# Optimization experiments

Measured on AMD Instinct MI355X. Metric: run time of the kernel, lower is better.

## Reference

```python
import jax, jax.numpy as jnp
import numpy as np

B, N, C = 128, 2048, 3
VL, PN = 256, 128  # vector_length, prediction_num
NEG_SLOPE = 0.01   # torch LeakyReLU default
BN_EPS = 1e-5


def _lin(key, fin, fout):
    k1, k2 = jax.random.split(key)
    lim = 1.0 / np.sqrt(fin)
    W = jax.random.uniform(k1, (fin, fout), minval=-lim, maxval=lim, dtype=jnp.float32)
    b = jax.random.uniform(k2, (fout,), minval=-lim, maxval=lim, dtype=jnp.float32)
    return W, b


def setup_inputs() -> dict:
    key = jax.random.key(0)
    ks = jax.random.split(key, 14)
    x = jax.random.normal(ks[0], (B, N, C), dtype=jnp.float32)
    lengths = jnp.maximum(jax.random.randint(ks[1], (B,), 0, N), 1).astype(jnp.int32)
    eps = jax.random.normal(ks[2], (B, VL), dtype=jnp.float32)
    W1, b1 = _lin(ks[3], C, 64)
    W2, b2 = _lin(ks[4], 64, 64)
    W3, b3 = _lin(ks[5], 64, 128)
    W4, b4 = _lin(ks[6], 128, 1024)
    Wf, bf = _lin(ks[7], 1024, 1024)
    Wmu, bmu = _lin(ks[8], 1024, VL)
    Wlv, blv = _lin(ks[9], 1024, VL)
    Wd1, bd1 = _lin(ks[10], VL, 1024)
    Wd2, bd2 = _lin(ks[11], 1024, 1024)
    Wd3, bd3 = _lin(ks[12], 1024, PN * C)
    g1 = jnp.ones((1024,), jnp.float32); be1 = jnp.zeros((1024,), jnp.float32)
    g2 = jnp.ones((1024,), jnp.float32); be2 = jnp.zeros((1024,), jnp.float32)
    return dict(x=x, lengths=lengths, eps=eps,
                W1=W1, b1=b1, W2=W2, b2=b2, W3=W3, b3=b3, W4=W4, b4=b4,
                Wf=Wf, bf=bf, Wmu=Wmu, bmu=bmu, Wlv=Wlv, blv=blv,
                Wd1=Wd1, bd1=bd1, g1=g1, be1=be1,
                Wd2=Wd2, bd2=bd2, g2=g2, be2=be2,
                Wd3=Wd3, bd3=bd3)


def _lrelu(h):
    return jnp.where(h > 0, h, NEG_SLOPE * h)


def _bn(h, g, b):
    # BatchNorm1d in training mode: biased batch stats
    m = h.mean(axis=0)
    v = h.var(axis=0)
    return (h - m) * jax.lax.rsqrt(v + BN_EPS) * g + b


def reference(x, lengths, eps,
              W1, b1, W2, b2, W3, b3, W4, b4,
              Wf, bf, Wmu, bmu, Wlv, blv,
              Wd1, bd1, g1, be1, Wd2, bd2, g2, be2, Wd3, bd3):
    # --- pointnet per-point MLP (batched over padded [B,N,C]) ---
    h = _lrelu(x @ W1 + b1)          # [B,N,64]
    h = _lrelu(h @ W2 + b2)          # [B,N,64]
    h = _lrelu(h @ W3 + b3)          # [B,N,128]
    h = _lrelu(h @ W4 + b4)          # [B,N,1024]
    # masked max over points (ragged -> padded+mask)
    mask = jnp.arange(N)[None, :] < lengths[:, None]   # [B,N]
    h = jnp.where(mask[:, :, None], h, -jnp.inf)
    pooled = jnp.max(h, axis=1)      # [B,1024]
    # --- encoder head ---
    e = _lrelu(pooled @ Wf + bf)
    mu = e @ Wmu + bmu               # [B,VL]
    logvar = e @ Wlv + blv           # [B,VL]
    # --- reparameterize ---
    z = mu + eps * jnp.exp(0.5 * logvar)
    # --- decoder: Linear+BN+LeakyReLU x2, final Linear ---
    d = _lrelu(_bn(z @ Wd1 + bd1, g1, be1))
    d = _lrelu(_bn(d @ Wd2 + bd2, g2, be2))
    y = (d @ Wd3 + bd3).reshape(-1, PN, C)   # [B,PN,C]
    return (y, mu, logvar)
```

## Files before the change

kernel.cpp:

```cpp
#include <hip/hip_runtime.h>
#include <hip/hip_bf16.h>
#include <math.h>

#define NEG_SLOPE 0.01f

typedef short short8 __attribute__((ext_vector_type(8)));
typedef float f32x4 __attribute__((ext_vector_type(4)));

__device__ __forceinline__ float lrelu(float v) { return v > 0.0f ? v : NEG_SLOPE * v; }

__device__ __forceinline__ short f2bf(float f) {
    __hip_bfloat16 h = __float2bfloat16(f);
    return __builtin_bit_cast(short, h);
}
__device__ __forceinline__ float bf2f(short s) {
    __hip_bfloat16 h = __builtin_bit_cast(__hip_bfloat16, s);
    return __bfloat162float(h);
}

__global__ __launch_bounds__(256) void pack_all(
    const float* __restrict__ W4, const float* __restrict__ Wf,
    const float* __restrict__ Wmu, const float* __restrict__ Wlv,
    const float* __restrict__ Wd1, const float* __restrict__ Wd2,
    const float* __restrict__ Wd3, const float* __restrict__ W2,
    const float* __restrict__ W3,
    short* __restrict__ F4, short* __restrict__ Ff, short* __restrict__ Fmuvl,
    short* __restrict__ Fd1, short* __restrict__ Fd2, short* __restrict__ Fd3,
    short* __restrict__ F2, short* __restrict__ F3)
{
    int bid = blockIdx.x;
    const float* src = nullptr; short* dst = nullptr; int K = 0, N = 0; int muvl = 0;
    if      (bid < 64)   { src = W4;  dst = F4;    K = 128;  N = 1024; }
    else if (bid < 576)  { src = Wf;  dst = Ff;    K = 1024; N = 1024; bid -= 64; }
    else if (bid < 832)  { src = nullptr; dst = Fmuvl; K = 1024; N = 512; muvl = 1; bid -= 576; }
    else if (bid < 960)  { src = Wd1; dst = Fd1;   K = 256;  N = 1024; bid -= 832; }
    else if (bid < 1472) { src = Wd2; dst = Fd2;   K = 1024; N = 1024; bid -= 960; }
    else if (bid < 1664) { src = Wd3; dst = Fd3;   K = 1024; N = 384;  bid -= 1472; }
    else if (bid < 1666) { src = W2;  dst = F2;    K = 64;   N = 64;   bid -= 1664; }
    else                 { src = W3;  dst = F3;    K = 64;   N = 128;  bid -= 1666; }

    const int fragid = bid * 4 + (threadIdx.x >> 6);
    const int lane   = threadIdx.x & 63;
    const int K32    = K >> 5;
    const int t   = fragid / (K32 * 4);
    const int rem = fragid - t * K32 * 4;
    const int ks  = rem >> 2;
    const int n   = rem & 3;
    const int col   = t * 64 + n * 16 + (lane & 15);
    const int kbase = ks * 32 + (lane >> 4) * 8;

    short8 v;
#pragma unroll
    for (int e = 0; e < 8; ++e) {
        float f;
        if (muvl) f = (col < 256) ? Wmu[(size_t)(kbase + e) * 256 + col]
                                  : Wlv[(size_t)(kbase + e) * 256 + col - 256];
        else      f = src[(size_t)(kbase + e) * N + col];
        v[e] = f2bf(f);
    }
    *(short8*)&dst[(size_t)fragid * 512 + lane * 8] = v;
}

__global__ __launch_bounds__(256, 2) void fused_pointnet_kernel(
    const float* __restrict__ x, const int* __restrict__ lengths,
    const float* __restrict__ W1, const float* __restrict__ b1,
    const float* __restrict__ b2, const float* __restrict__ b3,
    const short* __restrict__ F2, const short* __restrict__ F3,
    const short* __restrict__ F4,
    short* __restrict__ partials)
{
    const int tid = threadIdx.x;
    const int b   = blockIdx.x & 127;
    const int sc  = blockIdx.x >> 7;
    const int len = lengths[b];
    if (sc * 256 >= len) return;

    __shared__ short S[32768];
    const int lane = tid & 63;
    const int w    = tid >> 6;
    short* Aw = S + w * 8192;
    const int gid = b * 2048 + sc * 256 + tid;

    {
        const float x0 = x[gid * 3 + 0];
        const float x1 = x[gid * 3 + 1];
        const float x2 = x[gid * 3 + 2];
#pragma unroll
        for (int q = 0; q < 8; ++q) {
            short8 pv;
#pragma unroll
            for (int e = 0; e < 8; ++e) {
                int c = q * 8 + e;
                float v = b1[c];
                v = fmaf(x0, W1[c], v);
                v = fmaf(x1, W1[64 + c], v);
                v = fmaf(x2, W1[128 + c], v);
                pv[e] = f2bf(lrelu(v));
            }
            *(short8*)&Aw[lane * 64 + ((q ^ (lane & 7)) * 8)] = pv;
        }
    }

    {
        short8 a2[4][2];
#pragma unroll
        for (int m = 0; m < 4; ++m)
#pragma unroll
            for (int ks = 0; ks < 2; ++ks) {
                int rl = m * 16 + (lane & 15);
                int kch = ks * 4 + (lane >> 4);
                a2[m][ks] = *(const short8*)&Aw[rl * 64 + ((kch ^ (rl & 7)) * 8)];
            }
        short8 b2f[2][4];
#pragma unroll
        for (int ks = 0; ks < 2; ++ks)
#pragma unroll
            for (int n = 0; n < 4; ++n)
                b2f[ks][n] = *(const short8*)&F2[(size_t)(ks * 4 + n) * 512 + lane * 8];

        f32x4 acc2[4][4];
#pragma unroll
        for (int m = 0; m < 4; ++m)
#pragma unroll
            for (int n = 0; n < 4; ++n) acc2[m][n] = 0;
#pragma unroll
        for (int ks = 0; ks < 2; ++ks)
#pragma unroll
            for (int n = 0; n < 4; ++n)
#pragma unroll
                for (int m = 0; m < 4; ++m)
                    acc2[m][n] = __builtin_amdgcn_mfma_f32_16x16x32_bf16(
                        a2[m][ks], b2f[ks][n], acc2[m][n], 0, 0, 0);

#pragma unroll
        for (int n = 0; n < 4; ++n) {
            int col = n * 16 + (lane & 15);
            float bv = b2[col];
            int colch = col >> 3;
#pragma unroll
            for (int m = 0; m < 4; ++m)
#pragma unroll
                for (int r = 0; r < 4; ++r) {
                    int rl = m * 16 + (lane >> 4) * 4 + r;
                    Aw[4096 + rl * 64 + ((colch ^ (rl & 7)) * 8) + (col & 7)] =
                        f2bf(lrelu(acc2[m][n][r] + bv));
                }
        }
    }

    {
        short8 a3[4][2];
#pragma unroll
        for (int m = 0; m < 4; ++m)
#pragma unroll
            for (int ks = 0; ks < 2; ++ks) {
                int rl = m * 16 + (lane & 15);
                int kch = ks * 4 + (lane >> 4);
                a3[m][ks] = *(const short8*)&Aw[4096 + rl * 64 + ((kch ^ (rl & 7)) * 8)];
            }
#pragma unroll
        for (int half = 0; half < 2; ++half) {
            short8 b3f[2][4];
#pragma unroll
            for (int ks = 0; ks < 2; ++ks)
#pragma unroll
                for (int n = 0; n < 4; ++n)
                    b3f[ks][n] = *(const short8*)&F3[(size_t)(half * 8 + ks * 4 + n) * 512 + lane * 8];

            f32x4 acc3[4][4];
#pragma unroll
            for (int m = 0; m < 4; ++m)
#pragma unroll
                for (int n = 0; n < 4; ++n) acc3[m][n] = 0;
#pragma unroll
            for (int ks = 0; ks < 2; ++ks)
#pragma unroll
                for (int n = 0; n < 4; ++n)
#pragma unroll
                    for (int m = 0; m < 4; ++m)
                        acc3[m][n] = __builtin_amdgcn_mfma_f32_16x16x32_bf16(
                            a3[m][ks], b3f[ks][n], acc3[m][n], 0, 0, 0);

#pragma unroll
            for (int n = 0; n < 4; ++n) {
                int col = half * 64 + n * 16 + (lane & 15);
                float bv = b3[col];
                int colch = col >> 3;
#pragma unroll
                for (int m = 0; m < 4; ++m)
#pragma unroll
                    for (int r = 0; r < 4; ++r) {
                        int rl = m * 16 + (lane >> 4) * 4 + r;
                        Aw[rl * 128 + ((colch ^ (rl & 7)) * 8) + (col & 7)] =
                            f2bf(lrelu(acc3[m][n][r] + bv));
                    }
            }
        }
    }

    short8 af[4][4];
#pragma unroll
    for (int m = 0; m < 4; ++m)
#pragma unroll
        for (int ks = 0; ks < 4; ++ks) {
            int rl = m * 16 + (lane & 15);
            int ch = (ks * 4 + (lane >> 4)) ^ (rl & 7);
            af[m][ks] = *(const short8*)&Aw[rl * 128 + ch * 8];
        }

    const bool full = (sc * 256 + 256) <= len;
    float madd[4][4];
    if (!full) {
#pragma unroll
        for (int m = 0; m < 4; ++m)
#pragma unroll
            for (int r = 0; r < 4; ++r) {
                int rloc = sc * 256 + w * 64 + m * 16 + (lane >> 4) * 4 + r;
                madd[m][r] = (rloc < len) ? 0.0f : -INFINITY;
            }
    }

    short8 stg[4];
#pragma unroll
    for (int i = 0; i < 4; ++i)
        stg[i] = *(const short8*)&F4[w * 2048 + i * 512 + lane * 8];

    __syncthreads();
#pragma unroll
    for (int i = 0; i < 4; ++i)
        *(short8*)&S[w * 2048 + i * 512 + lane * 8] = stg[i];

    for (int t = 0; t < 16; ++t) {
        __syncthreads();
        if (t < 15) {
#pragma unroll
            for (int i = 0; i < 4; ++i)
                stg[i] = *(const short8*)&F4[(size_t)(t + 1) * 8192 + w * 2048 + i * 512 + lane * 8];
        }

        const short* Bb = S + (t & 1) * 8192;
        f32x4 acc[4][4];
#pragma unroll
        for (int m = 0; m < 4; ++m)
#pragma unroll
            for (int n = 0; n < 4; ++n) acc[m][n] = 0;

#pragma unroll
        for (int ks = 0; ks < 4; ++ks) {
            short8 bfr[4];
#pragma unroll
            for (int n = 0; n < 4; ++n)
                bfr[n] = *(const short8*)&Bb[(ks * 4 + n) * 512 + lane * 8];
#pragma unroll
            for (int n = 0; n < 4; ++n)
#pragma unroll
                for (int m = 0; m < 4; ++m)
                    acc[m][n] = __builtin_amdgcn_mfma_f32_16x16x32_bf16(
                        af[m][ks], bfr[n], acc[m][n], 0, 0, 0);
        }

        const size_t pb = ((size_t)((b * 8 + sc) * 4 + w)) * 1024 + t * 64;
#pragma unroll
        for (int n = 0; n < 4; ++n) {
            float v;
            if (full) {
                v = acc[0][n][0];
#pragma unroll
                for (int m = 0; m < 4; ++m)
#pragma unroll
                    for (int r = 0; r < 4; ++r)
                        if (m | r) v = fmaxf(v, acc[m][n][r]);
            } else {
                v = -INFINITY;
#pragma unroll
                for (int m = 0; m < 4; ++m)
#pragma unroll
                    for (int r = 0; r < 4; ++r)
                        v = fmaxf(v, acc[m][n][r] + madd[m][r]);
            }
            v = fmaxf(v, __shfl_xor(v, 16));
            v = fmaxf(v, __shfl_xor(v, 32));
            if (lane < 16) partials[pb + n * 16 + lane] = f2bf(v);
        }

        if (t < 15) {
            short* Bn = S + ((t + 1) & 1) * 8192;
#pragma unroll
            for (int i = 0; i < 4; ++i)
                *(short8*)&Bn[w * 2048 + i * 512 + lane * 8] = stg[i];
        }
    }
}

__global__ __launch_bounds__(256) void reduce_pool_kernel(
    const short* __restrict__ partials, const int* __restrict__ lengths,
    const float* __restrict__ b4, short* __restrict__ pooled)
{
    const int b = blockIdx.x;
    const int nlive = (lengths[b] + 255) >> 8;
    for (int i = threadIdx.x; i < 1024; i += 256) {
        float m = -INFINITY;
        for (int j = 0; j < nlive; ++j) {
#pragma unroll
            for (int w = 0; w < 4; ++w)
                m = fmaxf(m, bf2f(partials[((size_t)((b * 8 + j) * 4 + w)) * 1024 + i]));
        }
        pooled[(size_t)b * 1024 + i] = f2bf(lrelu(m + b4[i]));
    }
}

template<int MF, int K32>
__global__ __launch_bounds__(256) void gemm_tail(
    const short* __restrict__ A, const short* __restrict__ Wfrag,
    const float* __restrict__ bias,
    const float* __restrict__ g, const float* __restrict__ be,
    float* __restrict__ outF, short* __restrict__ outB,
    int Nout, int flags)
{
    __shared__ float bns[4][32];
    __shared__ float bnq[4][32];

    const int tid = threadIdx.x, lane = tid & 63, w = tid >> 6;
    const int K   = K32 * 32;
    const int c0  = blockIdx.x * 32;
    const int tt  = blockIdx.x >> 1;
    const int hf  = blockIdx.x & 1;
    const int row0  = (MF == 2) ? 0 : blockIdx.y * 64;
    const int arow0 = row0 + w * (MF * 16) + (lane & 15);
    const int koff  = (lane >> 4) * 8;

    f32x4 acc[MF][2];
#pragma unroll
    for (int m = 0; m < MF; ++m) { acc[m][0] = 0; acc[m][1] = 0; }

#pragma unroll
    for (int ks = 0; ks < K32; ++ks) {
        short8 a[MF], bfr[2];
#pragma unroll
        for (int m = 0; m < MF; ++m)
            a[m] = *(const short8*)&A[(size_t)(arow0 + m * 16) * K + ks * 32 + koff];
#pragma unroll
        for (int n = 0; n < 2; ++n)
            bfr[n] = *(const short8*)&Wfrag[(size_t)((tt * K32 + ks) * 4 + hf * 2 + n) * 512 + lane * 8];
#pragma unroll
        for (int n = 0; n < 2; ++n)
#pragma unroll
            for (int m = 0; m < MF; ++m)
                acc[m][n] = __builtin_amdgcn_mfma_f32_16x16x32_bf16(a[m], bfr[n], acc[m][n], 0, 0, 0);
    }

    if ((flags & 2) && MF == 2) {
#pragma unroll
        for (int n = 0; n < 2; ++n) {
            float s = 0.f, q = 0.f;
#pragma unroll
            for (int m = 0; m < MF; ++m)
#pragma unroll
                for (int r = 0; r < 4; ++r) {
                    float v = acc[m][n][r];
                    s += v; q = fmaf(v, v, q);
                }
            s += __shfl_xor(s, 16); s += __shfl_xor(s, 32);
            q += __shfl_xor(q, 16); q += __shfl_xor(q, 32);
            if (lane < 16) { bns[w][n * 16 + lane] = s; bnq[w][n * 16 + lane] = q; }
        }
        __syncthreads();
#pragma unroll
        for (int n = 0; n < 2; ++n) {
            int cl = n * 16 + (lane & 15);
            float s = bns[0][cl] + bns[1][cl] + bns[2][cl] + bns[3][cl];
            float q = bnq[0][cl] + bnq[1][cl] + bnq[2][cl] + bnq[3][cl];
            float mean = s * (1.0f / 128.0f);
            float var  = q * (1.0f / 128.0f) - mean * mean;
            float rs   = 1.0f / sqrtf(var + 1e-5f);
            float gg   = g[c0 + cl] * rs;
            float bb   = be[c0 + cl] - mean * gg;
#pragma unroll
            for (int m = 0; m < MF; ++m)
#pragma unroll
                for (int r = 0; r < 4; ++r)
                    acc[m][n][r] = fmaf(acc[m][n][r], gg, bb);
        }
    } else if (bias) {
#pragma unroll
        for (int n = 0; n < 2; ++n) {
            float bv = bias[c0 + n * 16 + (lane & 15)];
#pragma unroll
            for (int m = 0; m < MF; ++m)
#pragma unroll
                for (int r = 0; r < 4; ++r) acc[m][n][r] += bv;
        }
    }

    if (flags & 1) {
#pragma unroll
        for (int m = 0; m < MF; ++m)
#pragma unroll
            for (int n = 0; n < 2; ++n)
#pragma unroll
                for (int r = 0; r < 4; ++r) acc[m][n][r] = lrelu(acc[m][n][r]);
    }

#pragma unroll
    for (int m = 0; m < MF; ++m)
#pragma unroll
        for (int n = 0; n < 2; ++n)
#pragma unroll
            for (int r = 0; r < 4; ++r) {
                int row = row0 + w * (MF * 16) + m * 16 + (lane >> 4) * 4 + r;
                int col = c0 + n * 16 + (lane & 15);
                if (flags & 4) outB[(size_t)row * Nout + col] = f2bf(acc[m][n][r]);
                else           outF[(size_t)row * Nout + col] = acc[m][n][r];
            }
}

__global__ __launch_bounds__(256) void gemm_muvlz(
    const short* __restrict__ A, const short* __restrict__ Fmuvl,
    const float* __restrict__ bmu, const float* __restrict__ blv,
    const float* __restrict__ eps,
    float* __restrict__ mu_out, float* __restrict__ lv_out,
    short* __restrict__ zbuf)
{
    const int tid = threadIdx.x, lane = tid & 63, w = tid >> 6;
    const int c0 = blockIdx.x * 32;
    const int tt = blockIdx.x >> 1;
    const int hf = blockIdx.x & 1;
    const int row0 = blockIdx.y * 64;
    const int arow = row0 + w * 16 + (lane & 15);
    const int koff = (lane >> 4) * 8;

    f32x4 macc[2], lacc[2];
#pragma unroll
    for (int n = 0; n < 2; ++n) { macc[n] = 0; lacc[n] = 0; }

#pragma unroll
    for (int ks = 0; ks < 32; ++ks) {
        short8 a = *(const short8*)&A[(size_t)arow * 1024 + ks * 32 + koff];
#pragma unroll
        for (int n = 0; n < 2; ++n) {
            short8 bm = *(const short8*)&Fmuvl[(size_t)((tt * 32 + ks) * 4 + hf * 2 + n) * 512 + lane * 8];
            short8 bl = *(const short8*)&Fmuvl[(size_t)(((tt + 4) * 32 + ks) * 4 + hf * 2 + n) * 512 + lane * 8];
            macc[n] = __builtin_amdgcn_mfma_f32_16x16x32_bf16(a, bm, macc[n], 0, 0, 0);
            lacc[n] = __builtin_amdgcn_mfma_f32_16x16x32_bf16(a, bl, lacc[n], 0, 0, 0);
        }
    }

#pragma unroll
    for (int n = 0; n < 2; ++n) {
        int col = c0 + n * 16 + (lane & 15);
        float bmv = bmu[col], blvv = blv[col];
#pragma unroll
        for (int r = 0; r < 4; ++r) {
            int row = row0 + w * 16 + (lane >> 4) * 4 + r;
            float mu = macc[n][r] + bmv;
            float lv = lacc[n][r] + blvv;
            mu_out[(size_t)row * 256 + col] = mu;
            lv_out[(size_t)row * 256 + col] = lv;
            float z = fmaf(eps[(size_t)row * 256 + col], expf(0.5f * lv), mu);
            zbuf[(size_t)row * 256 + col] = f2bf(z);
        }
    }
}

extern "C" void kernel_launch(void* const* d_in, const int* in_sizes, int n_in,
                              void* d_out, int out_size, void* d_ws, size_t ws_size,
                              hipStream_t stream)
{
    const float* x       = (const float*)d_in[0];
    const int*   lengths = (const int*)  d_in[1];
    const float* eps     = (const float*)d_in[2];
    const float* W1  = (const float*)d_in[3];  const float* b1  = (const float*)d_in[4];
    const float* W2  = (const float*)d_in[5];  const float* b2  = (const float*)d_in[6];
    const float* W3  = (const float*)d_in[7];  const float* b3  = (const float*)d_in[8];
    const float* W4  = (const float*)d_in[9];  const float* b4  = (const float*)d_in[10];
    const float* Wf  = (const float*)d_in[11]; const float* bf  = (const float*)d_in[12];
    const float* Wmu = (const float*)d_in[13]; const float* bmu = (const float*)d_in[14];
    const float* Wlv = (const float*)d_in[15]; const float* blv = (const float*)d_in[16];
    const float* Wd1 = (const float*)d_in[17];
    const float* g1  = (const float*)d_in[19]; const float* be1 = (const float*)d_in[20];
    const float* Wd2 = (const float*)d_in[21];
    const float* g2  = (const float*)d_in[23]; const float* be2 = (const float*)d_in[24];
    const float* Wd3 = (const float*)d_in[25]; const float* bd3 = (const float*)d_in[26];

    float* out = (float*)d_out;
    float* y_out  = out;
    float* mu_out = out + 49152;
    float* lv_out = out + 81920;

    char* ws = (char*)d_ws;
    short* F4    = (short*)(ws + 0);
    short* Ff    = (short*)(ws + 262144);
    short* Fmuvl = (short*)(ws + 2359296);
    short* Fd1   = (short*)(ws + 3407872);
    short* Fd2   = (short*)(ws + 3932160);
    short* Fd3   = (short*)(ws + 6029312);
    short* F2    = (short*)(ws + 6815744);
    short* F3    = (short*)(ws + 6823936);
    short* partials = (short*)(ws + 6840320);
    short* pooled = (short*)(ws + 15228928);
    short* ebuf   = (short*)(ws + 15491072);
    short* zbuf   = (short*)(ws + 15753216);
    short* d1v    = (short*)(ws + 15818752);
    short* d2v    = (short*)(ws + 16080896);

    pack_all<<<1670, 256, 0, stream>>>(W4, Wf, Wmu, Wlv, Wd1, Wd2, Wd3, W2, W3,
                                       F4, Ff, Fmuvl, Fd1, Fd2, Fd3, F2, F3);
    fused_pointnet_kernel<<<1024, 256, 0, stream>>>(
        x, lengths, W1, b1, b2, b3, F2, F3, F4, partials);
    reduce_pool_kernel<<<128, 256, 0, stream>>>(partials, lengths, b4, pooled);
    gemm_tail<1, 32><<<dim3(32, 2), 256, 0, stream>>>(pooled, Ff, bf, nullptr, nullptr,
                                                      nullptr, ebuf, 1024, 1 | 4);
    gemm_muvlz<<<dim3(8, 2), 256, 0, stream>>>(ebuf, Fmuvl, bmu, blv, eps,
                                               mu_out, lv_out, zbuf);
    gemm_tail<2, 8><<<32, 256, 0, stream>>>(zbuf, Fd1, nullptr, g1, be1,
                                            nullptr, d1v, 1024, 1 | 2 | 4);
    gemm_tail<2, 32><<<32, 256, 0, stream>>>(d1v, Fd2, nullptr, g2, be2,
                                             nullptr, d2v, 1024, 1 | 2 | 4);
    gemm_tail<1, 32><<<dim3(12, 2), 256, 0, stream>>>(d2v, Fd3, bd3, nullptr, nullptr,
                                                      y_out, nullptr, 384, 0);
}
```

Before: 144.2 us.

## Split pointnet into h3 materialization and weight-stationary layer4 max-pool kernel

The fused per-point kernel is split in two. The first kernel computes layers 1-3 per 64-point group and writes the 128-wide activations to global memory in MFMA fragment order. The second kernel keeps a 32-column slice of W4 in registers per wave, streams all of a batch's activation chunks, and takes the running max directly, which removes the partials buffer and the separate reduce kernel. In exchange, the h3 intermediate (about 64MB) makes an extra round trip through global memory, and each activation chunk is reread by every column-wave.

```diff
diff --git a/kernel.cpp b/kernel.cpp
--- a/kernel.cpp
+++ b/kernel.cpp
@@ -61,25 +61,25 @@
     *(short8*)&dst[(size_t)fragid * 512 + lane * 8] = v;
 }
 
-__global__ __launch_bounds__(256, 2) void fused_pointnet_kernel(
+__global__ __launch_bounds__(128, 2) void h3_kernel(
     const float* __restrict__ x, const int* __restrict__ lengths,
     const float* __restrict__ W1, const float* __restrict__ b1,
     const float* __restrict__ b2, const float* __restrict__ b3,
     const short* __restrict__ F2, const short* __restrict__ F3,
-    const short* __restrict__ F4,
-    short* __restrict__ partials)
+    short* __restrict__ h3p)
 {
-    const int tid = threadIdx.x;
-    const int b   = blockIdx.x & 127;
-    const int sc  = blockIdx.x >> 7;
-    const int len = lengths[b];
-    if (sc * 256 >= len) return;
-
-    __shared__ short S[32768];
+    const int tid  = threadIdx.x;
+    const int b    = blockIdx.x & 127;
+    const int c2   = blockIdx.x >> 7;
     const int lane = tid & 63;
     const int w    = tid >> 6;
+    const int g    = c2 * 2 + w;
+    const int len  = lengths[b];
+    if (g * 64 >= len) return;
+
+    __shared__ short S[16384];
     short* Aw = S + w * 8192;
-    const int gid = b * 2048 + sc * 256 + tid;
+    const int gid = b * 2048 + g * 64 + lane;
 
     {
         const float x0 = x[gid * 3 + 0];
@@ -198,114 +198,118 @@
         }
     }
 
-    short8 af[4][4];
-#pragma unroll
-    for (int m = 0; m < 4; ++m)
-#pragma unroll
-        for (int ks = 0; ks < 4; ++ks) {
+    const size_t obase = ((size_t)(b * 32 + g) * 16) * 512 + lane * 8;
+#pragma unroll
+    for (int ks = 0; ks < 4; ++ks)
+#pragma unroll
+        for (int m = 0; m < 4; ++m) {
             int rl = m * 16 + (lane & 15);
             int ch = (ks * 4 + (lane >> 4)) ^ (rl & 7);
-            af[m][ks] = *(const short8*)&Aw[rl * 128 + ch * 8];
-        }
-
-    const bool full = (sc * 256 + 256) <= len;
-    float madd[4][4];
-    if (!full) {
-#pragma unroll
-        for (int m = 0; m < 4; ++m)
-#pragma unroll
-            for (int r = 0; r < 4; ++r) {
-                int rloc = sc * 256 + w * 64 + m * 16 + (lane >> 4) * 4 + r;
-                madd[m][r] = (rloc < len) ? 0.0f : -INFINITY;
-            }
-    }
-
-    short8 stg[4];
-#pragma unroll
-    for (int i = 0; i < 4; ++i)
-        stg[i] = *(const short8*)&F4[w * 2048 + i * 512 + lane * 8];
-
-    __syncthreads();
-#pragma unroll
-    for (int i = 0; i < 4; ++i)
-        *(short8*)&S[w * 2048 + i * 512 + lane * 8] = stg[i];
-
-    for (int t = 0; t < 16; ++t) {
-        __syncthreads();
-        if (t < 15) {
-#pragma unroll
-            for (int i = 0; i < 4; ++i)
-                stg[i] = *(const short8*)&F4[(size_t)(t + 1) * 8192 + w * 2048 + i * 512 + lane * 8];
-        }
-
-        const short* Bb = S + (t & 1) * 8192;
-        f32x4 acc[4][4];
-#pragma unroll
-        for (int m = 0; m < 4; ++m)
-#pragma unroll
-            for (int n = 0; n < 4; ++n) acc[m][n] = 0;
-
+            short8 af = *(const short8*)&Aw[rl * 128 + ch * 8];
+            *(short8*)&h3p[obase + (size_t)(ks * 4 + m) * 512] = af;
+        }
+}
+
+__global__ __launch_bounds__(512, 4) void l4_pool_kernel(
+    const short* __restrict__ h3p, const int* __restrict__ lengths,
+    const short* __restrict__ F4, const float* __restrict__ b4,
+    short* __restrict__ pooled)
+{
+    const int tid = threadIdx.x, lane = tid & 63, w = tid >> 6;
+    const int b   = blockIdx.x;
+    const int cb  = blockIdx.y;
+    const int len = lengths[b];
+    const int c0  = cb * 256 + w * 32;
+    const int t   = c0 >> 6;
+    const int n0  = (c0 >> 4) & 3;
+
+    short8 bfr[4][2];
+#pragma unroll
+    for (int ks = 0; ks < 4; ++ks)
+#pragma unroll
+        for (int n = 0; n < 2; ++n)
+            bfr[ks][n] = *(const short8*)&F4[(size_t)((t * 4 + ks) * 4 + n0 + n) * 512 + lane * 8];
+
+    const int nfull = len >> 6;
+    const int rem   = len & 63;
+
+    f32x4 rmax[2];
+#pragma unroll
+    for (int n = 0; n < 2; ++n)
+#pragma unroll
+        for (int r = 0; r < 4; ++r) rmax[n][r] = -INFINITY;
+
+    const size_t arow = (size_t)b * 32;
+    for (int c = 0; c < nfull; ++c) {
+        const size_t ab = (arow + c) * 16 * 512 + lane * 8;
+        f32x4 acc[4][2];
+#pragma unroll
+        for (int m = 0; m < 4; ++m) { acc[m][0] = 0; acc[m][1] = 0; }
 #pragma unroll
         for (int ks = 0; ks < 4; ++ks) {
-            short8 bfr[4];
-#pragma unroll
-            for (int n = 0; n < 4; ++n)
-                bfr[n] = *(const short8*)&Bb[(ks * 4 + n) * 512 + lane * 8];
-#pragma unroll
-            for (int n = 0; n < 4; ++n)
+            short8 a[4];
+#pragma unroll
+            for (int m = 0; m < 4; ++m)
+                a[m] = *(const short8*)&h3p[ab + (size_t)(ks * 4 + m) * 512];
+#pragma unroll
+            for (int n = 0; n < 2; ++n)
 #pragma unroll
                 for (int m = 0; m < 4; ++m)
                     acc[m][n] = __builtin_amdgcn_mfma_f32_16x16x32_bf16(
-                        af[m][ks], bfr[n], acc[m][n], 0, 0, 0);
-        }
-
-        const size_t pb = ((size_t)((b * 8 + sc) * 4 + w)) * 1024 + t * 64;
-#pragma unroll
-        for (int n = 0; n < 4; ++n) {
-            float v;
-            if (full) {
-                v = acc[0][n][0];
+                        a[m], bfr[ks][n], acc[m][n], 0, 0, 0);
+        }
+#pragma unroll
+        for (int n = 0; n < 2; ++n)
+#pragma unroll
+            for (int m = 0; m < 4; ++m)
+#pragma unroll
+                for (int r = 0; r < 4; ++r)
+                    rmax[n][r] = fmaxf(rmax[n][r], acc[m][n][r]);
+    }
+
+    if (rem) {
+        float madd[4][4];
+#pragma unroll
+        for (int m = 0; m < 4; ++m)
+#pragma unroll
+            for (int r = 0; r < 4; ++r)
+                madd[m][r] = (m * 16 + (lane >> 4) * 4 + r < rem) ? 0.0f : -INFINITY;
+
+        const size_t ab = (arow + nfull) * 16 * 512 + lane * 8;
+        f32x4 acc[4][2];
+#pragma unroll
+        for (int m = 0; m < 4; ++m) { acc[m][0] = 0; acc[m][1] = 0; }
+#pragma unroll
+        for (int ks = 0; ks < 4; ++ks) {
+            short8 a[4];
+#pragma unroll
+            for (int m = 0; m < 4; ++m)
+                a[m] = *(const short8*)&h3p[ab + (size_t)(ks * 4 + m) * 512];
+#pragma unroll
+            for (int n = 0; n < 2; ++n)
 #pragma unroll
                 for (int m = 0; m < 4; ++m)
-#pragma unroll
-                    for (int r = 0; r < 4; ++r)
-                        if (m | r) v = fmaxf(v, acc[m][n][r]);
-            } else {
-                v = -INFINITY;
-#pragma unroll
-                for (int m = 0; m < 4; ++m)
-#pragma unroll
-                    for (int r = 0; r < 4; ++r)
-                        v = fmaxf(v, acc[m][n][r] + madd[m][r]);
-            }
-            v = fmaxf(v, __shfl_xor(v, 16));
-            v = fmaxf(v, __shfl_xor(v, 32));
-            if (lane < 16) partials[pb + n * 16 + lane] = f2bf(v);
-        }
-
-        if (t < 15) {
-            short* Bn = S + ((t + 1) & 1) * 8192;
-#pragma unroll
-            for (int i = 0; i < 4; ++i)
-                *(short8*)&Bn[w * 2048 + i * 512 + lane * 8] = stg[i];
-        }
-    }
-}
-
-__global__ __launch_bounds__(256) void reduce_pool_kernel(
-    const short* __restrict__ partials, const int* __restrict__ lengths,
-    const float* __restrict__ b4, short* __restrict__ pooled)
-{
-    const int b = blockIdx.x;
-    const int nlive = (lengths[b] + 255) >> 8;
-    for (int i = threadIdx.x; i < 1024; i += 256) {
-        float m = -INFINITY;
-        for (int j = 0; j < nlive; ++j) {
-#pragma unroll
-            for (int w = 0; w < 4; ++w)
-                m = fmaxf(m, bf2f(partials[((size_t)((b * 8 + j) * 4 + w)) * 1024 + i]));
-        }
-        pooled[(size_t)b * 1024 + i] = f2bf(lrelu(m + b4[i]));
+                    acc[m][n] = __builtin_amdgcn_mfma_f32_16x16x32_bf16(
+                        a[m], bfr[ks][n], acc[m][n], 0, 0, 0);
+        }
+#pragma unroll
+        for (int n = 0; n < 2; ++n)
+#pragma unroll
+            for (int m = 0; m < 4; ++m)
+#pragma unroll
+                for (int r = 0; r < 4; ++r)
+                    rmax[n][r] = fmaxf(rmax[n][r], acc[m][n][r] + madd[m][r]);
+    }
+
+#pragma unroll
+    for (int n = 0; n < 2; ++n) {
+        float v = fmaxf(fmaxf(rmax[n][0], rmax[n][1]),
+                        fmaxf(rmax[n][2], rmax[n][3]));
+        v = fmaxf(v, __shfl_xor(v, 16));
+        v = fmaxf(v, __shfl_xor(v, 32));
+        int col = c0 + n * 16 + (lane & 15);
+        if (lane < 16)
+            pooled[(size_t)b * 1024 + col] = f2bf(lrelu(v + b4[col]));
     }
 }
 
@@ -496,18 +500,19 @@
     short* Fd3   = (short*)(ws + 6029312);
     short* F2    = (short*)(ws + 6815744);
     short* F3    = (short*)(ws + 6823936);
-    short* partials = (short*)(ws + 6840320);
-    short* pooled = (short*)(ws + 15228928);
-    short* ebuf   = (short*)(ws + 15491072);
-    short* zbuf   = (short*)(ws + 15753216);
-    short* d1v    = (short*)(ws + 15818752);
-    short* d2v    = (short*)(ws + 16080896);
+    short* h3p   = (short*)(ws + 6840320);
+    short* pooled = (short*)(ws + 73949184);
+    short* ebuf   = (short*)(ws + 74211328);
+    short* zbuf   = (short*)(ws + 74473472);
+    short* d1v    = (short*)(ws + 74539008);
+    short* d2v    = (short*)(ws + 74801152);
 
     pack_all<<<1670, 256, 0, stream>>>(W4, Wf, Wmu, Wlv, Wd1, Wd2, Wd3, W2, W3,
                                        F4, Ff, Fmuvl, Fd1, Fd2, Fd3, F2, F3);
-    fused_pointnet_kernel<<<1024, 256, 0, stream>>>(
-        x, lengths, W1, b1, b2, b3, F2, F3, F4, partials);
-    reduce_pool_kernel<<<128, 256, 0, stream>>>(partials, lengths, b4, pooled);
+    h3_kernel<<<2048, 128, 0, stream>>>(
+        x, lengths, W1, b1, b2, b3, F2, F3, h3p);
+    l4_pool_kernel<<<dim3(128, 4), 512, 0, stream>>>(
+        h3p, lengths, F4, b4, pooled);
     gemm_tail<1, 32><<<dim3(32, 2), 256, 0, stream>>>(pooled, Ff, bf, nullptr, nullptr,
                                                       nullptr, ebuf, 1024, 1 | 4);
     gemm_muvlz<<<dim3(8, 2), 256, 0, stream>>>(ebuf, Fmuvl, bmu, blv, eps,
```

Result: slower. 153.2 us (+6.2%).
